# Kernel optimization log

Hardware: AMD Instinct MI355X
Metric: run time of the kernel (lower is better)

## Reference

```python
import jax, jax.numpy as jnp
import numpy as np

R = 128          # input voxel grid resolution
N = 200000
C_IN = 128
C_OUT = 256
G = 32           # group-norm groups
EPS = 1e-5


def _build_sparse_structure():
    """Generate random sparse voxel coords, downsample map, and 3x3x3 neighbor table."""
    rng = np.random.default_rng(0)
    lin = rng.choice(R ** 3, size=N, replace=False)
    cx, cy, cz = lin // (R * R), (lin // R) % R, lin % R
    # downsample by 2: coords // 2 on a (R//2)^3 grid
    Rd = R // 2
    key = ((cx // 2) * Rd + (cy // 2)) * Rd + (cz // 2)
    uk, inv = np.unique(key, return_inverse=True)   # uk sorted
    M = len(uk)
    dx, dy, dz = uk // (Rd * Rd), (uk // Rd) % Rd, uk % Rd
    # 27-neighbor table for submanifold 3x3x3 conv on the downsampled coords
    nbr = np.full((M, 27), -1, np.int32)
    k = 0
    for ox in (-1, 0, 1):
        for oy in (-1, 0, 1):
            for oz in (-1, 0, 1):
                nx, ny, nz = dx + ox, dy + oy, dz + oz
                valid = (nx >= 0) & (nx < Rd) & (ny >= 0) & (ny < Rd) & (nz >= 0) & (nz < Rd)
                nkey = (nx * Rd + ny) * Rd + nz
                pos = np.clip(np.searchsorted(uk, nkey), 0, M - 1)
                found = valid & (uk[pos] == nkey)
                nbr[:, k] = np.where(found, pos, -1).astype(np.int32)
                k += 1
    return inv.astype(np.int32), nbr, M


def setup_inputs() -> dict:
    pool_seg, nbr_idx, M = _build_sparse_structure()
    key = jax.random.key(0)
    ks = jax.random.split(key, 12)
    f32 = jnp.float32
    feats = jax.random.normal(ks[0], (N, C_IN), f32)
    s1 = float(1.0 / np.sqrt(27 * C_IN))
    s2 = float(1.0 / np.sqrt(27 * C_OUT))
    return {
        "feats": feats,
        "gn1_w": 1.0 + 0.1 * jax.random.normal(ks[1], (C_IN,), f32),
        "gn1_b": 0.1 * jax.random.normal(ks[2], (C_IN,), f32),
        "W1": jax.random.normal(ks[3], (27, C_IN, C_OUT), f32) * s1,
        "b1": 0.01 * jax.random.normal(ks[4], (C_OUT,), f32),
        "gn2_w": 1.0 + 0.1 * jax.random.normal(ks[5], (C_OUT,), f32),
        "gn2_b": 0.1 * jax.random.normal(ks[6], (C_OUT,), f32),
        "W2": jax.random.normal(ks[7], (27, C_OUT, C_OUT), f32) * s2,
        "b2": 0.01 * jax.random.normal(ks[8], (C_OUT,), f32),
        "Wskip": jax.random.normal(ks[9], (C_IN, C_OUT), f32) * float(1.0 / np.sqrt(C_IN)),
        "bskip": 0.01 * jax.random.normal(ks[10], (C_OUT,), f32),
        "pool_seg": jnp.asarray(pool_seg),
        "nbr_idx": jnp.asarray(nbr_idx),
        "num_down": int(M),
    }


def _group_norm(x, gamma, beta):
    # batch size 1: normalize each group over all voxels and its channels
    n, c = x.shape
    xg = x.reshape(n, G, c // G)
    mu = xg.mean(axis=(0, 2), keepdims=True)
    var = xg.var(axis=(0, 2), keepdims=True)
    xn = (xg - mu) * jax.lax.rsqrt(var + EPS)
    return xn.reshape(n, c) * gamma + beta


def _sparse_conv3(x, W, b, nbr_idx):
    # submanifold 3x3x3 conv: out[i] = sum_k W[k] @ x[nbr[i,k]] (missing nbr -> 0)
    idx = jnp.maximum(nbr_idx, 0)
    mask = (nbr_idx >= 0).astype(x.dtype)
    acc = jnp.zeros((x.shape[0], W.shape[2]), x.dtype)
    for k in range(27):
        acc = acc + (x[idx[:, k]] * mask[:, k:k + 1]) @ W[k]
    return acc + b


def reference(feats, gn1_w, gn1_b, W1, b1, gn2_w, gn2_b, W2, b2, Wskip, bskip,
              pool_seg, nbr_idx, num_down):
    # act_layers: GroupNorm32 + SiLU on the full-resolution sparse tensor
    h = jax.nn.silu(_group_norm(feats, gn1_w, gn1_b))
    # SparseDownsample(2): average features of voxels sharing a coord//2 cell
    cnt = jax.ops.segment_sum(jnp.ones((feats.shape[0], 1), feats.dtype),
                              pool_seg, num_segments=num_down)
    inv_cnt = 1.0 / jnp.maximum(cnt, 1.0)
    h_d = jax.ops.segment_sum(h, pool_seg, num_segments=num_down) * inv_cnt
    x_d = jax.ops.segment_sum(feats, pool_seg, num_segments=num_down) * inv_cnt
    # out_layers: conv3 -> GN -> SiLU -> conv3
    h1 = _sparse_conv3(h_d, W1, b1, nbr_idx)
    h2 = jax.nn.silu(_group_norm(h1, gn2_w, gn2_b))
    h3 = _sparse_conv3(h2, W2, b2, nbr_idx)
    # skip: 1x1 sparse conv on downsampled input, then add (same coord set)
    skip = x_d @ Wskip + bskip
    return h3 + skip
```

## Files before the change

kernel.cpp:

```cpp
#include <hip/hip_runtime.h>
#include <hip/hip_bf16.h>
#include <stdint.h>

typedef __hip_bfloat16 bf16;
typedef __attribute__((ext_vector_type(8))) __bf16 bf16x8;
typedef __attribute__((ext_vector_type(4))) float f32x4;

#define GN_EPS 1e-5f

__device__ __forceinline__ float silu_f(float x) {
  return x / (1.f + __expf(-x));
}

__device__ __forceinline__ float ldf(const void* p, size_t i, int f) {
  return f ? ((const float*)p)[i]
           : __bfloat162float(((const bf16*)p)[i]);
}

__device__ __forceinline__ void llds16(const void* g, void* l) {
  __builtin_amdgcn_global_load_lds(
      (const __attribute__((address_space(1))) unsigned int*)g,
      (__attribute__((address_space(3))) unsigned int*)l, 16, 0, 0);
}

__device__ __forceinline__ void gload16(bf16x8& d, const bf16* base, int voff) {
  asm volatile("global_load_dwordx4 %0, %1, %2"
               : "=&v"(d) : "v"(voff), "s"(base) : "memory");
}

__global__ void detect_k(const void* __restrict__ gn1w, int* __restrict__ flag) {
  if (threadIdx.x == 0 && blockIdx.x == 0) {
    const unsigned short* u = (const unsigned short*)gn1w;
    float mx = 0.f;
    for (int i = 0; i < 128; ++i) {
      unsigned int b = ((unsigned int)u[i]) << 16;
      float v = __uint_as_float(b);
      v = fabsf(v);
      if (!isnan(v) && v > mx) mx = v;
    }
    flag[0] = (mx > 1e4f) ? 1 : 0;
  }
}

__global__ void transpose_k(const void* __restrict__ in, bf16* __restrict__ out,
                            int CI, int CO, const int* __restrict__ flagp) {
  const int f = *flagp;
  int k = blockIdx.y;
  int ntco = CO >> 5;
  int tci = blockIdx.x / ntco, tco = blockIdx.x % ntco;
  __shared__ float t[32][33];
  int tx = threadIdx.x & 31, ty = threadIdx.x >> 5;
  size_t base = (size_t)k * CI * CO;
  bf16* dst = out + base;
#pragma unroll
  for (int j = 0; j < 4; ++j)
    t[ty + 8 * j][tx] =
        ldf(in, base + (size_t)(tci * 32 + ty + 8 * j) * CO + tco * 32 + tx, f);
  __syncthreads();
#pragma unroll
  for (int j = 0; j < 4; ++j)
    dst[(size_t)tci * (CO * 32) + (size_t)(tco * 32 + ty + 8 * j) * 32 + tx] =
        __float2bfloat16(t[tx][ty + 8 * j]);
}

__global__ void gn_stats_k(const void* __restrict__ x, float* __restrict__ raw,
                           int rows, int C, const int* __restrict__ flagp) {
  const int f = *flagp;
  int tid = threadIdx.x;
  int rpb = 256 / C;
  int c = tid & (C - 1);
  int stripe = tid / C;
  float s = 0.f, sq = 0.f;
  for (int r = blockIdx.x * rpb + stripe; r < rows; r += gridDim.x * rpb) {
    float v = ldf(x, (size_t)r * C + c, f);
    s += v; sq += v * v;
  }
  __shared__ float ls[256], lq[256];
  ls[tid] = s; lq[tid] = sq;
  __syncthreads();
  if (tid < 32) {
    int per = C >> 5;
    float as = 0.f, aq = 0.f;
    for (int st = 0; st < rpb; ++st)
      for (int e = 0; e < per; ++e) {
        int idx = st * C + tid * per + e;
        as += ls[idx]; aq += lq[idx];
      }
    atomicAdd(&raw[tid], as);
    atomicAdd(&raw[32 + tid], aq);
  }
}

__global__ void gn_fin_k(const float* __restrict__ raw, float* __restrict__ fin,
                         float count) {
  int g = threadIdx.x;
  if (g < 32) {
    float mu = raw[g] / count;
    float var = fmaxf(raw[32 + g] / count - mu * mu, 0.f);
    fin[g] = mu;
    fin[32 + g] = rsqrtf(var + GN_EPS);
  }
}

__global__ void slots_k(const int* __restrict__ seg, int* __restrict__ cnt,
                        int* __restrict__ slots, int N) {
  int i = blockIdx.x * 256 + threadIdx.x;
  if (i >= N) return;
  int s = seg[i];
  int p = atomicAdd(&cnt[s], 1);
  if (p < 8) slots[s * 8 + p] = i;
}

__global__ void down_k(const void* __restrict__ feats, const int* __restrict__ slots,
                       const int* __restrict__ cnt, const float* __restrict__ fin1,
                       const void* __restrict__ gw, const void* __restrict__ gb,
                       bf16* __restrict__ xd, bf16* __restrict__ hd, int M,
                       const int* __restrict__ flagp) {
  const int f = *flagp;
  int cell = blockIdx.x * 2 + (threadIdx.x >> 7);
  int c = threadIdx.x & 127;
  if (cell >= M) return;
  int n = min(cnt[cell], 8);
  int g = c >> 2;
  float mu = fin1[g], is = fin1[32 + g];
  float w = ldf(gw, c, f), b = ldf(gb, c, f);
  float xs = 0.f, hs = 0.f;
  for (int j = 0; j < n; ++j) {
    int v = slots[cell * 8 + j];
    float fv = ldf(feats, (size_t)v * 128 + c, f);
    xs += fv;
    hs += silu_f((fv - mu) * is * w + b);
  }
  float inv = 1.f / (float)max(n, 1);
  xd[(size_t)cell * 128 + c] = __float2bfloat16(xs * inv);
  hd[(size_t)cell * 128 + c] = __float2bfloat16(hs * inv);
}

__global__ void act2_k(bf16* __restrict__ h, const float* __restrict__ fin2,
                       const void* __restrict__ gw, const void* __restrict__ gb,
                       size_t total8, const int* __restrict__ flagp) {
  const int f = *flagp;
  size_t i = (size_t)blockIdx.x * 256 + threadIdx.x;
  if (i >= total8) return;
  int c0 = (int)((i * 8) & 255);
  int g = c0 >> 3;
  float mu = fin2[g], is = fin2[32 + g];
  bf16x8 v = *reinterpret_cast<bf16x8*>(h + i * 8);
  bf16x8 o;
#pragma unroll
  for (int j = 0; j < 8; ++j) {
    float x = (float)v[j];
    float t = (x - mu) * is * ldf(gw, c0 + j, f) + ldf(gb, c0 + j, f);
    o[j] = (__bf16)silu_f(t);
  }
  *reinterpret_cast<bf16x8*>(h + i * 8) = o;
}

template <int CIN, bool SKIP>
__global__ __launch_bounds__(512, 2) void conv_k(
    const bf16* __restrict__ A, const bf16* __restrict__ Wt,
    const void* __restrict__ bias, const void* __restrict__ bias2,
    const bf16* __restrict__ Xd, const int* __restrict__ nbr,
    void* __restrict__ out, int M, int nwg, const void* __restrict__ zp,
    const int* __restrict__ biasflagp, const int* __restrict__ outflagp) {
  constexpr int NCB = CIN / 32;
  constexpr int LOG_NCB = (CIN == 256) ? 3 : 2;
  constexpr int NT = 27 * NCB + (SKIP ? 4 : 0);
  __shared__ alignas(16) char smem[49152 + 27648];
  char* Aring = smem;
  int* nbrT = (int*)(smem + 49152);

  const int bflag = *biasflagp, oflag = *outflagp;
  const int tid = threadIdx.x;
  const int wave = tid >> 6, lane = tid & 63;
  const bool w03 = (wave < 4);

  int bid = blockIdx.x;
  int q = nwg >> 3, r8 = nwg & 7, xcd = bid & 7, ix = bid >> 3;
  int wg = (xcd < r8 ? xcd * (q + 1) : r8 * (q + 1) + (xcd - r8) * q) + ix;
  const int row0 = wg * 192;

  for (int i = tid; i < 27 * 256; i += 512) {
    int k = i >> 8, r = i & 255;
    int g = row0 + r;
    int v = -1;
    if (r < 192 && g < M) v = nbr[(size_t)g * 27 + k];
    nbrT[i] = v;
  }
  __syncthreads();

  const int srow = lane >> 2;
  const int schk = lane & 3;

  auto stageA1 = [&](int t, int panel, char* Asl, bool isW, int kk, int koff,
                     int cink, const bf16* Ab) {
    int r = panel * 16 + srow;
    int src;
    if (isW) src = nbrT[(kk << 8) + r];
    else { int g = row0 + r; src = (g < M) ? g : -1; }
    int lc = schk ^ ((r >> 1) & 3);
    const bf16* ga = (src >= 0) ? Ab + (size_t)src * cink + koff + lc * 8
                                : (const bf16*)zp;
    llds16(ga, Asl + (size_t)panel * 1024);
  };

  auto stageA = [&](int t) {
    char* Asl = Aring + (size_t)(t & 3) * 12288;
    const bool isW = (!SKIP) || (t < 27 * NCB);
    const int kk = t >> LOG_NCB;
    const int cb = isW ? (t & (NCB - 1)) : (t - 27 * NCB);
    const int cink = isW ? CIN : 128;
    const bf16* Ab = isW ? A : Xd;
    const int koff = cb * 32;
    if (w03) {
      stageA1(t, 2 * wave, Asl, isW, kk, koff, cink, Ab);
      stageA1(t, 2 * wave + 1, Asl, isW, kk, koff, cink, Ab);
    } else {
      stageA1(t, 4 + wave, Asl, isW, kk, koff, cink, Ab);
    }
  };

  const int mrow = lane & 15, quad = lane >> 4;
  const int wr = wave >> 2, wc = wave & 3;
  const int cswz = (quad ^ ((mrow >> 1) & 3)) * 16;

  int bvoff[4];
#pragma unroll
  for (int j = 0; j < 4; ++j)
    bvoff[j] = ((wc * 64 + j * 16 + mrow) * 32 + quad * 8) * 2;

  auto loadB = [&](bf16x8 (&dst)[4], int t) {
    const bool isW = (!SKIP) || (t < 27 * NCB);
    const int kk = t >> LOG_NCB;
    const int cb = isW ? (t & (NCB - 1)) : (t - 27 * NCB);
    const bf16* base = Wt +
        (isW ? (size_t)kk * (256 * CIN) : (size_t)27 * (256 * CIN)) +
        (size_t)cb * (256 * 32);
#pragma unroll
    for (int j = 0; j < 4; ++j) gload16(dst[j], base, bvoff[j]);
  };

  f32x4 acc[6][4] = {};

  auto compute = [&](int t, const bf16x8 (&bv)[4]) {
    const char* As = Aring + (size_t)(t & 3) * 12288 +
                     (size_t)(wr * 96 + mrow) * 64 + cswz;
    bf16x8 af[6];
#pragma unroll
    for (int i = 0; i < 6; ++i)
      af[i] = *reinterpret_cast<const bf16x8*>(As + i * (16 * 64));
    __builtin_amdgcn_s_setprio(1);
#pragma unroll
    for (int i = 0; i < 6; ++i)
#pragma unroll
      for (int j = 0; j < 4; ++j)
        acc[i][j] = __builtin_amdgcn_mfma_f32_16x16x32_bf16(af[i], bv[j],
                                                            acc[i][j], 0, 0, 0);
    __builtin_amdgcn_s_setprio(0);
  };

#define VMW(a, b)                                                        \
  do {                                                                   \
    if (w03) asm volatile("s_waitcnt vmcnt(" #a ")" ::: "memory");       \
    else     asm volatile("s_waitcnt vmcnt(" #b ")" ::: "memory");       \
    __builtin_amdgcn_sched_barrier(0);                                   \
  } while (0)
#define BAR() __builtin_amdgcn_s_barrier()

  bf16x8 bX[4], bY[4];

  stageA(0); stageA(1);
  loadB(bX, 0);

#pragma unroll 1
  for (int u = 0; u < NT / 2 - 1; ++u) {
    const int s = 2 * u;
    loadB(bY, s + 1);
    stageA(s + 2);
    VMW(6, 5);
    BAR();
    compute(s, bX);
    loadB(bX, s + 2);
    stageA(s + 3);
    VMW(8, 6);
    BAR();
    compute(s + 1, bY);
  }
  loadB(bY, NT - 1);
  VMW(6, 5);
  BAR();
  compute(NT - 2, bX);
  VMW(0, 0);
  BAR();
  compute(NT - 1, bY);

#undef VMW
#undef BAR

#pragma unroll
  for (int j = 0; j < 4; ++j) {
    int col = wc * 64 + j * 16 + mrow;
    float bvl = ldf(bias, col, bflag);
    if (SKIP) bvl += ldf(bias2, col, bflag);
#pragma unroll
    for (int i = 0; i < 6; ++i) {
      int rb = row0 + wr * 96 + i * 16 + quad * 4;
#pragma unroll
      for (int r = 0; r < 4; ++r) {
        int row = rb + r;
        if (row < M) {
          size_t idx = (size_t)row * 256 + col;
          float val = acc[i][j][r] + bvl;
          if (oflag) ((float*)out)[idx] = val;
          else ((bf16*)out)[idx] = __float2bfloat16(val);
        }
      }
    }
  }
}

extern "C" void kernel_launch(void* const* d_in, const int* in_sizes, int n_in,
                              void* d_out, int out_size, void* d_ws, size_t ws_size,
                              hipStream_t stream) {
  const void* feats = d_in[0];
  const void* gn1w = d_in[1];
  const void* gn1b = d_in[2];
  const void* W1 = d_in[3];
  const void* b1 = d_in[4];
  const void* gn2w = d_in[5];
  const void* gn2b = d_in[6];
  const void* W2 = d_in[7];
  const void* b2 = d_in[8];
  const void* Wsk = d_in[9];
  const void* bsk = d_in[10];
  const int* pool = (const int*)d_in[11];
  const int* nbr = (const int*)d_in[12];
  const int N = in_sizes[0] / 128;
  const int M = out_size / 256;

  char* ws = (char*)d_ws;
  auto aup = [](size_t x) { return (x + 255) & ~(size_t)255; };
  float* raw1 = (float*)(ws + 0);
  float* raw2 = (float*)(ws + 256);
  int* flag = (int*)(ws + 512);
  int* zeroflag = (int*)(ws + 516);
  const void* zp = (const void*)(ws + 768);
  int* cnt = (int*)(ws + 1024);
  size_t o = aup(1024 + (size_t)M * 4);
  float* fin1 = (float*)(ws + o); o += 256;
  float* fin2 = (float*)(ws + o); o += 256;
  int* slots = (int*)(ws + o); o = aup(o + (size_t)M * 32);
  bf16* xd = (bf16*)(ws + o); o += (size_t)M * 256;
  bf16* hd = (bf16*)(ws + o); o += (size_t)M * 256;
  bf16* h1 = (bf16*)(ws + o); o += (size_t)M * 512;
  bf16* wt1 = (bf16*)(ws + o); o += (size_t)27 * 256 * 128 * 2;
  bf16* wt2 = (bf16*)(ws + o); o += ((size_t)27 * 256 * 256 + 256 * 128) * 2;
  (void)ws_size; (void)n_in;

  hipMemsetAsync(ws, 0, 1024 + (size_t)M * 4, stream);

  detect_k<<<1, 64, 0, stream>>>(gn1w, flag);

  transpose_k<<<dim3(4 * 8, 27), 256, 0, stream>>>(W1, wt1, 128, 256, flag);
  transpose_k<<<dim3(8 * 8, 27), 256, 0, stream>>>(W2, wt2, 256, 256, flag);
  transpose_k<<<dim3(4 * 8, 1), 256, 0, stream>>>(
      Wsk, wt2 + (size_t)27 * 256 * 256, 128, 256, flag);

  gn_stats_k<<<512, 256, 0, stream>>>(feats, raw1, N, 128, flag);
  gn_fin_k<<<1, 64, 0, stream>>>(raw1, fin1, (float)N * 4.f);

  slots_k<<<(N + 255) / 256, 256, 0, stream>>>(pool, cnt, slots, N);
  down_k<<<(M + 1) / 2, 256, 0, stream>>>(feats, slots, cnt, fin1, gn1w, gn1b,
                                          xd, hd, M, flag);

  const int nwg = (M + 191) / 192;

  conv_k<128, false><<<nwg, 512, 0, stream>>>(
      hd, wt1, b1, nullptr, nullptr, nbr, h1, M, nwg, zp, flag, zeroflag);

  gn_stats_k<<<512, 256, 0, stream>>>(h1, raw2, M, 256, zeroflag);
  gn_fin_k<<<1, 64, 0, stream>>>(raw2, fin2, (float)M * 8.f);
  act2_k<<<(int)(((size_t)M * 32 + 255) / 256), 256, 0, stream>>>(
      h1, fin2, gn2w, gn2b, (size_t)M * 32, flag);

  conv_k<256, true><<<nwg, 512, 0, stream>>>(
      h1, wt2, b2, bsk, xd, nbr, d_out, M, nwg, zp, flag, flag);
}
```

Measured before the change: 1.375 ms.

## Halve conv row tile to 96 rows per workgroup and simplify A staging

The conv kernel's per-workgroup row tile shrinks from 192 to 96 rows, so each wave accumulates 3 instead of 6 M-fragments and LDS use drops to about 35KB. A-tile staging is now done by six waves with one 16-row panel each instead of eight waves covering twelve panels, and the vmcnt waits are retuned to match. B loads switch to flat 64-bit addressing instead of SGPR base plus VGPR offset. This doubles the number of workgroups and lowers per-block LDS and registers for more occupancy. In exchange, each B weight fragment loaded from global memory is reused across half as many rows, roughly doubling weight traffic.

```diff
diff --git a/kernel.cpp b/kernel.cpp
--- a/kernel.cpp
+++ b/kernel.cpp
@@ -23,9 +23,9 @@
       (__attribute__((address_space(3))) unsigned int*)l, 16, 0, 0);
 }
 
-__device__ __forceinline__ void gload16(bf16x8& d, const bf16* base, int voff) {
-  asm volatile("global_load_dwordx4 %0, %1, %2"
-               : "=&v"(d) : "v"(voff), "s"(base) : "memory");
+__device__ __forceinline__ void gload16(bf16x8& d, const bf16* addr) {
+  asm volatile("global_load_dwordx4 %0, %1, off"
+               : "=&v"(d) : "v"(addr) : "memory");
 }
 
 __global__ void detect_k(const void* __restrict__ gn1w, int* __restrict__ flag) {
@@ -166,25 +166,25 @@
   constexpr int NCB = CIN / 32;
   constexpr int LOG_NCB = (CIN == 256) ? 3 : 2;
   constexpr int NT = 27 * NCB + (SKIP ? 4 : 0);
-  __shared__ alignas(16) char smem[49152 + 27648];
+  __shared__ alignas(16) char smem[24576 + 10368];
   char* Aring = smem;
-  int* nbrT = (int*)(smem + 49152);
+  int* nbrT = (int*)(smem + 24576);
 
   const int bflag = *biasflagp, oflag = *outflagp;
   const int tid = threadIdx.x;
   const int wave = tid >> 6, lane = tid & 63;
-  const bool w03 = (wave < 4);
+  const bool wlo = (wave < 6);
 
   int bid = blockIdx.x;
   int q = nwg >> 3, r8 = nwg & 7, xcd = bid & 7, ix = bid >> 3;
   int wg = (xcd < r8 ? xcd * (q + 1) : r8 * (q + 1) + (xcd - r8) * q) + ix;
-  const int row0 = wg * 192;
-
-  for (int i = tid; i < 27 * 256; i += 512) {
-    int k = i >> 8, r = i & 255;
+  const int row0 = wg * 96;
+
+  for (int i = tid; i < 27 * 96; i += 512) {
+    int k = i / 96, r = i - k * 96;
     int g = row0 + r;
     int v = -1;
-    if (r < 192 && g < M) v = nbr[(size_t)g * 27 + k];
+    if (g < M) v = nbr[(size_t)g * 27 + k];
     nbrT[i] = v;
   }
   __syncthreads();
@@ -192,42 +192,33 @@
   const int srow = lane >> 2;
   const int schk = lane & 3;
 
-  auto stageA1 = [&](int t, int panel, char* Asl, bool isW, int kk, int koff,
-                     int cink, const bf16* Ab) {
-    int r = panel * 16 + srow;
-    int src;
-    if (isW) src = nbrT[(kk << 8) + r];
-    else { int g = row0 + r; src = (g < M) ? g : -1; }
-    int lc = schk ^ ((r >> 1) & 3);
-    const bf16* ga = (src >= 0) ? Ab + (size_t)src * cink + koff + lc * 8
-                                : (const bf16*)zp;
-    llds16(ga, Asl + (size_t)panel * 1024);
-  };
-
   auto stageA = [&](int t) {
-    char* Asl = Aring + (size_t)(t & 3) * 12288;
+    if (!wlo) return;
+    char* Asl = Aring + (size_t)(t & 3) * 6144;
     const bool isW = (!SKIP) || (t < 27 * NCB);
     const int kk = t >> LOG_NCB;
     const int cb = isW ? (t & (NCB - 1)) : (t - 27 * NCB);
     const int cink = isW ? CIN : 128;
     const bf16* Ab = isW ? A : Xd;
     const int koff = cb * 32;
-    if (w03) {
-      stageA1(t, 2 * wave, Asl, isW, kk, koff, cink, Ab);
-      stageA1(t, 2 * wave + 1, Asl, isW, kk, koff, cink, Ab);
-    } else {
-      stageA1(t, 4 + wave, Asl, isW, kk, koff, cink, Ab);
-    }
+    int r = wave * 16 + srow;
+    int src;
+    if (isW) src = nbrT[kk * 96 + r];
+    else { int g = row0 + r; src = (g < M) ? g : -1; }
+    int lc = schk ^ ((r >> 1) & 3);
+    const bf16* ga = (src >= 0) ? Ab + (size_t)src * cink + koff + lc * 8
+                                : (const bf16*)zp;
+    llds16(ga, Asl + (size_t)wave * 1024);
   };
 
   const int mrow = lane & 15, quad = lane >> 4;
   const int wr = wave >> 2, wc = wave & 3;
   const int cswz = (quad ^ ((mrow >> 1) & 3)) * 16;
 
-  int bvoff[4];
+  int beoff[4];
 #pragma unroll
   for (int j = 0; j < 4; ++j)
-    bvoff[j] = ((wc * 64 + j * 16 + mrow) * 32 + quad * 8) * 2;
+    beoff[j] = (wc * 64 + j * 16 + mrow) * 32 + quad * 8;
 
   auto loadB = [&](bf16x8 (&dst)[4], int t) {
     const bool isW = (!SKIP) || (t < 27 * NCB);
@@ -237,21 +228,21 @@
         (isW ? (size_t)kk * (256 * CIN) : (size_t)27 * (256 * CIN)) +
         (size_t)cb * (256 * 32);
 #pragma unroll
-    for (int j = 0; j < 4; ++j) gload16(dst[j], base, bvoff[j]);
+    for (int j = 0; j < 4; ++j) gload16(dst[j], base + beoff[j]);
   };
 
-  f32x4 acc[6][4] = {};
+  f32x4 acc[3][4] = {};
 
   auto compute = [&](int t, const bf16x8 (&bv)[4]) {
-    const char* As = Aring + (size_t)(t & 3) * 12288 +
-                     (size_t)(wr * 96 + mrow) * 64 + cswz;
-    bf16x8 af[6];
-#pragma unroll
-    for (int i = 0; i < 6; ++i)
+    const char* As = Aring + (size_t)(t & 3) * 6144 +
+                     (size_t)(wr * 48 + mrow) * 64 + cswz;
+    bf16x8 af[3];
+#pragma unroll
+    for (int i = 0; i < 3; ++i)
       af[i] = *reinterpret_cast<const bf16x8*>(As + i * (16 * 64));
     __builtin_amdgcn_s_setprio(1);
 #pragma unroll
-    for (int i = 0; i < 6; ++i)
+    for (int i = 0; i < 3; ++i)
 #pragma unroll
       for (int j = 0; j < 4; ++j)
         acc[i][j] = __builtin_amdgcn_mfma_f32_16x16x32_bf16(af[i], bv[j],
@@ -261,7 +252,7 @@
 
 #define VMW(a, b)                                                        \
   do {                                                                   \
-    if (w03) asm volatile("s_waitcnt vmcnt(" #a ")" ::: "memory");       \
+    if (wlo) asm volatile("s_waitcnt vmcnt(" #a ")" ::: "memory");       \
     else     asm volatile("s_waitcnt vmcnt(" #b ")" ::: "memory");       \
     __builtin_amdgcn_sched_barrier(0);                                   \
   } while (0)
@@ -277,17 +268,17 @@
     const int s = 2 * u;
     loadB(bY, s + 1);
     stageA(s + 2);
-    VMW(6, 5);
+    VMW(5, 4);
     BAR();
     compute(s, bX);
     loadB(bX, s + 2);
     stageA(s + 3);
-    VMW(8, 6);
+    VMW(6, 4);
     BAR();
     compute(s + 1, bY);
   }
   loadB(bY, NT - 1);
-  VMW(6, 5);
+  VMW(4, 4);
   BAR();
   compute(NT - 2, bX);
   VMW(0, 0);
@@ -303,8 +294,8 @@
     float bvl = ldf(bias, col, bflag);
     if (SKIP) bvl += ldf(bias2, col, bflag);
 #pragma unroll
-    for (int i = 0; i < 6; ++i) {
-      int rb = row0 + wr * 96 + i * 16 + quad * 4;
+    for (int i = 0; i < 3; ++i) {
+      int rb = row0 + wr * 48 + i * 16 + quad * 4;
 #pragma unroll
       for (int r = 0; r < 4; ++r) {
         int row = rb + r;
@@ -373,7 +364,7 @@
   down_k<<<(M + 1) / 2, 256, 0, stream>>>(feats, slots, cnt, fin1, gn1w, gn1b,
                                           xd, hd, M, flag);
 
-  const int nwg = (M + 191) / 192;
+  const int nwg = (M + 95) / 96;
 
   conv_k<128, false><<<nwg, 512, 0, stream>>>(
       hd, wt1, b1, nullptr, nullptr, nbr, h1, M, nwg, zp, flag, zeroflag);
```

After: 1.652 ms. +20.2%, slower.
